# Kernel tuning notes

Hardware: AMD Instinct MI355X
Metric: run time of the kernel (lower is better)

## Reference

```python
import jax, jax.numpy as jnp
import numpy as np

BS, NQ, NK = 4096, 21, 7   # batch, num_neg queries, 7 keys (weekdays)
E = 512                     # key_size == query_size
H = 512                     # hidden_size
NEG_INF = -1e9


def setup_inputs() -> dict:
    key = jax.random.key(0)
    ks = jax.random.split(key, 6)
    sq = 1.0 / np.sqrt(E)
    sh = 1.0 / np.sqrt(H)
    return {
        "queries": jax.random.normal(ks[0], (BS, NQ, E), jnp.float32),
        "keys": jax.random.normal(ks[1], (BS, NK, E), jnp.float32),
        "wq_w": jax.random.normal(ks[2], (H, E), jnp.float32) * sq,
        "wq_b": jnp.zeros((H,), jnp.float32),
        "wk_w": jax.random.normal(ks[3], (H, E), jnp.float32) * sq,
        "wk_b": jnp.zeros((H,), jnp.float32),
        "wv_w": jax.random.normal(ks[4], (1, H), jnp.float32) * sh,
        "wv_b": jnp.zeros((1,), jnp.float32),
        "cum_subs_masks": jax.random.randint(ks[5], (BS, 1, NK, 1), 0, 2).astype(jnp.int32),
        "num_neg": NQ,
    }


def reference(queries, keys, wq_w, wq_b, wk_w, wk_b, wv_w, wv_b, cum_subs_masks, num_neg):
    # dropout p=0.0 -> identity (as in eval / p=0)
    q = jnp.einsum('bqe,he->bqh', queries, wq_w) + wq_b          # (bs,21,H)
    k = jnp.einsum('bke,he->bkh', keys, wk_w) + wk_b             # (bs,7,H)
    # additive score: broadcast q over keys, k over queries
    t = jnp.tanh(q[:, :, None, :] + k[:, None, :, :])            # (bs,21,7,H)
    scores = jnp.einsum('bqkh,oh->bqko', t, wv_w) + wv_b         # (bs,21,7,1)
    scores = scores + cum_subs_masks.astype(scores.dtype) * NEG_INF
    attn_weights = jax.nn.softmax(scores, axis=-2)               # softmax over 7 keys
    # weighted sum of the RAW keys (the module multiplies by expanded `keys`)
    attn_out = jnp.einsum('bqk,bke->bqe', attn_weights[..., 0], keys)  # (bs,21,E)
    return (attn_out, attn_weights)
```

## Files before the change

kernel.cpp:

```cpp
#include <hip/hip_runtime.h>

#define BS_   4096
#define NQ_   21
#define NK_   7
#define E_    512
#define MQ_   (BS_*NQ_)
#define MK_   (BS_*NK_)
#define SCALE_ 2.88539008177792681f

typedef __attribute__((ext_vector_type(8))) short bf16x8;
typedef __attribute__((ext_vector_type(4))) float f32x4;
typedef __attribute__((ext_vector_type(8))) unsigned short u16x8;

__device__ __forceinline__ unsigned int cvt_pk_bf16(float lo, float hi){
  unsigned int r;
  asm("v_cvt_pk_bf16_f32 %0, %1, %2" : "=v"(r) : "v"(lo), "v"(hi));
  return r;
}
__device__ __forceinline__ float bf2f(unsigned short h){
  return __builtin_bit_cast(float, (unsigned int)h << 16);
}
__device__ __forceinline__ void gload_lds16(const void* g, void* l){
  __builtin_amdgcn_global_load_lds(
      (const __attribute__((address_space(1))) unsigned int*)g,
      (__attribute__((address_space(3))) unsigned int*)l, 16, 0, 0);
}

__global__ __launch_bounds__(256) void cast_weights(
    const float* __restrict__ wq, const float* __restrict__ wk,
    unsigned int* __restrict__ oq, unsigned int* __restrict__ ok)
{
  int i = blockIdx.x * 256 + threadIdx.x;
  float4 a = ((const float4*)wq)[i];
  float4 b = ((const float4*)wk)[i];
  uint2 ua = { cvt_pk_bf16(a.x, a.y), cvt_pk_bf16(a.z, a.w) };
  uint2 ub = { cvt_pk_bf16(b.x, b.y), cvt_pk_bf16(b.z, b.w) };
  ((uint2*)oq)[i] = ua;
  ((uint2*)ok)[i] = ub;
}

__global__ __launch_bounds__(256, 2)
void gemm_proj(const float* __restrict__ A, const unsigned short* __restrict__ Bw,
               const float* __restrict__ bias, unsigned short* __restrict__ C, int M)
{
  __shared__ unsigned short Asm[2][128 * 64];
  __shared__ unsigned short Bsm[2][128 * 64];

  const int tid  = threadIdx.x;
  const int lane = tid & 63;
  const int w    = tid >> 6;
  const int wr   = w >> 1, wc = w & 1;

  const int nwg = (M >> 7) << 2;
  int bid = (int)blockIdx.x;
  const int q8 = nwg >> 3;
  bid = (bid & 7) * q8 + (bid >> 3);
  const int  mt = bid >> 2, nt = bid & 3;
  const long m0 = (long)mt << 7;
  const int  n0 = nt << 7;

  const int a_row = tid >> 4;
  const int a_c4  = tid & 15;
  const float* Abase = A + m0 * E_;

  f32x4 acc[4][4];
  const f32x4 z4 = {0.f, 0.f, 0.f, 0.f};
#pragma unroll
  for (int m = 0; m < 4; ++m)
#pragma unroll
    for (int n = 0; n < 4; ++n) acc[m][n] = z4;

  {
#pragma unroll
    for (int i = 0; i < 4; ++i){
      const int tb  = (w << 12) + (i << 10) + (lane << 4);
      const int row = tb >> 7, cb = tb & 127;
      gload_lds16((const char*)Bw + ((n0 + row) << 10) + cb,
                  (char*)Bsm[0] + (w << 12) + (i << 10));
    }
    float4 av[8];
#pragma unroll
    for (int j = 0; j < 8; ++j)
      av[j] = *(const float4*)(Abase + (long)(a_row + j * 16) * E_ + a_c4 * 4);
#pragma unroll
    for (int j = 0; j < 8; ++j){
      uint2 u = { cvt_pk_bf16(av[j].x, av[j].y), cvt_pk_bf16(av[j].z, av[j].w) };
      *(uint2*)&Asm[0][(a_row + j * 16) * 64 + a_c4 * 4] = u;
    }
  }
  __syncthreads();

#pragma unroll
  for (int t = 0; t < 8; ++t){
    const int buf = t & 1, nbuf = buf ^ 1;
    float4 av[8];
    if (t < 7){
      const int k0 = (t + 1) << 6;
#pragma unroll
      for (int i = 0; i < 4; ++i){
        const int tb  = (w << 12) + (i << 10) + (lane << 4);
        const int row = tb >> 7, cb = tb & 127;
        gload_lds16((const char*)Bw + ((n0 + row) << 10) + (k0 << 1) + cb,
                    (char*)Bsm[nbuf] + (w << 12) + (i << 10));
      }
#pragma unroll
      for (int j = 0; j < 8; ++j)
        av[j] = *(const float4*)(Abase + (long)(a_row + j * 16) * E_ + k0 + a_c4 * 4);
    }
#pragma unroll
    for (int kk = 0; kk < 2; ++kk){
      bf16x8 af[4], bfr[4];
#pragma unroll
      for (int m = 0; m < 4; ++m)
        af[m] = *(const bf16x8*)&Asm[buf][(wr * 64 + m * 16 + (lane & 15)) * 64 + kk * 32 + (lane >> 4) * 8];
#pragma unroll
      for (int n = 0; n < 4; ++n)
        bfr[n] = *(const bf16x8*)&Bsm[buf][(wc * 64 + n * 16 + (lane & 15)) * 64 + kk * 32 + (lane >> 4) * 8];
#pragma unroll
      for (int m = 0; m < 4; ++m)
#pragma unroll
        for (int n = 0; n < 4; ++n)
          acc[m][n] = __builtin_amdgcn_mfma_f32_16x16x32_bf16(af[m], bfr[n], acc[m][n], 0, 0, 0);
    }
    if (t < 7){
#pragma unroll
      for (int j = 0; j < 8; ++j){
        uint2 u = { cvt_pk_bf16(av[j].x, av[j].y), cvt_pk_bf16(av[j].z, av[j].w) };
        *(uint2*)&Asm[nbuf][(a_row + j * 16) * 64 + a_c4 * 4] = u;
      }
    }
    __syncthreads();
  }

  const int ccol0 = n0 + wc * 64 + (lane & 15);
  float bvs[4];
#pragma unroll
  for (int n = 0; n < 4; ++n) bvs[n] = bias[ccol0 + n * 16] * SCALE_;
#pragma unroll
  for (int m = 0; m < 4; ++m){
    const long rbase = m0 + wr * 64 + m * 16 + (lane >> 4) * 4;
#pragma unroll
    for (int n = 0; n < 4; ++n){
      const long col = ccol0 + n * 16;
      float v0 = fmaf(acc[m][n][0], SCALE_, bvs[n]);
      float v1 = fmaf(acc[m][n][1], SCALE_, bvs[n]);
      float v2 = fmaf(acc[m][n][2], SCALE_, bvs[n]);
      float v3 = fmaf(acc[m][n][3], SCALE_, bvs[n]);
      unsigned int u01 = cvt_pk_bf16(v0, v1);
      unsigned int u23 = cvt_pk_bf16(v2, v3);
      C[(rbase + 0) * E_ + col] = (unsigned short)(u01 & 0xffffu);
      C[(rbase + 1) * E_ + col] = (unsigned short)(u01 >> 16);
      C[(rbase + 2) * E_ + col] = (unsigned short)(u23 & 0xffffu);
      C[(rbase + 3) * E_ + col] = (unsigned short)(u23 >> 16);
    }
  }
}

__global__ __launch_bounds__(256, 2)
void attn_fused(const unsigned short* __restrict__ qp,
                const unsigned short* __restrict__ kp,
                const float* __restrict__ keys,
                const float* __restrict__ wv, const float* __restrict__ wvb,
                const int* __restrict__ mask,
                float* __restrict__ out0, float* __restrict__ out1)
{
  const int lane = threadIdx.x & 63;
  const int b    = blockIdx.x * 4 + (threadIdx.x >> 6);

  float wvr[8];
  *(float4*)&wvr[0] = ((const float4*)wv)[lane * 2];
  *(float4*)&wvr[4] = ((const float4*)wv)[lane * 2 + 1];

  float kf[NK_][8];
#pragma unroll
  for (int k = 0; k < NK_; ++k){
    u16x8 u = *(const u16x8*)(kp + ((long)b * NK_ + k) * E_ + lane * 8);
#pragma unroll
    for (int j = 0; j < 8; ++j) kf[k][j] = bf2f((unsigned short)u[j]);
  }
  float kr[NK_][8];
#pragma unroll
  for (int k = 0; k < NK_; ++k){
    const float4* p = (const float4*)(keys + ((long)b * NK_ + k) * E_ + lane * 8);
    *(float4*)&kr[k][0] = p[0];
    *(float4*)&kr[k][4] = p[1];
  }

  float wsum = ((wvr[0] + wvr[1]) + (wvr[2] + wvr[3])) + ((wvr[4] + wvr[5]) + (wvr[6] + wvr[7]));
#pragma unroll
  for (int off = 32; off; off >>= 1) wsum += __shfl_xor(wsum, off, 64);

  const float vb = wvb[0];
  float base[NK_];
#pragma unroll
  for (int k = 0; k < NK_; ++k)
    base[k] = (wsum + vb) + (float)mask[b * NK_ + k] * (-1e9f);

  const unsigned short* qrow = qp + (long)b * NQ_ * E_ + lane * 8;
  u16x8 qv = *(const u16x8*)qrow;

  float4* o0 = (float4*)(out0 + (long)b * NQ_ * E_) + lane * 2;
  float*  o1 = out1 + (long)b * (NQ_ * NK_);

  for (int qi = 0; qi < NQ_; ++qi){
    u16x8 qn = qv;
    if (qi < NQ_ - 1) qn = *(const u16x8*)(qrow + (qi + 1) * E_);

    float qf[8];
#pragma unroll
    for (int j = 0; j < 8; ++j) qf[j] = bf2f((unsigned short)qv[j]);
    qv = qn;

    float acc[NK_];
#pragma unroll
    for (int k = 0; k < NK_; ++k){
      float a = 0.f;
#pragma unroll
      for (int j = 0; j < 8; ++j){
        float x = qf[j] + kf[k][j];
        float e = __builtin_amdgcn_exp2f(x);
        float r = __builtin_amdgcn_rcpf(e + 1.0f);
        a = fmaf(wvr[j], r, a);
      }
      acc[k] = a;
    }
#pragma unroll
    for (int k = 0; k < NK_; ++k){
      float a = acc[k];
#pragma unroll
      for (int off = 32; off; off >>= 1) a += __shfl_xor(a, off, 64);
      acc[k] = a;
    }
    float sc[NK_], mx = -3.4e38f;
#pragma unroll
    for (int k = 0; k < NK_; ++k){ sc[k] = fmaf(-2.f, acc[k], base[k]); mx = fmaxf(mx, sc[k]); }
    float sum = 0.f;
#pragma unroll
    for (int k = 0; k < NK_; ++k){ sc[k] = __expf(sc[k] - mx); sum += sc[k]; }
    const float inv = __builtin_amdgcn_rcpf(sum);
    float wgt[NK_];
#pragma unroll
    for (int k = 0; k < NK_; ++k) wgt[k] = sc[k] * inv;

    float wsel = wgt[0];
#pragma unroll
    for (int k = 1; k < NK_; ++k) wsel = (lane == k) ? wgt[k] : wsel;
    if (lane < NK_) o1[qi * NK_ + lane] = wsel;

    float4 lo = {0.f,0.f,0.f,0.f}, hi = {0.f,0.f,0.f,0.f};
#pragma unroll
    for (int k = 0; k < NK_; ++k){
      lo.x = fmaf(wgt[k], kr[k][0], lo.x);
      lo.y = fmaf(wgt[k], kr[k][1], lo.y);
      lo.z = fmaf(wgt[k], kr[k][2], lo.z);
      lo.w = fmaf(wgt[k], kr[k][3], lo.w);
      hi.x = fmaf(wgt[k], kr[k][4], hi.x);
      hi.y = fmaf(wgt[k], kr[k][5], hi.y);
      hi.z = fmaf(wgt[k], kr[k][6], hi.z);
      hi.w = fmaf(wgt[k], kr[k][7], hi.w);
    }
    o0[qi * 128 + 0] = lo;
    o0[qi * 128 + 1] = hi;
  }
}

extern "C" void kernel_launch(void* const* d_in, const int* in_sizes, int n_in,
                              void* d_out, int out_size, void* d_ws, size_t ws_size,
                              hipStream_t stream)
{
  const float* queries = (const float*)d_in[0];
  const float* keys    = (const float*)d_in[1];
  const float* wq_w    = (const float*)d_in[2];
  const float* wq_b    = (const float*)d_in[3];
  const float* wk_w    = (const float*)d_in[4];
  const float* wk_b    = (const float*)d_in[5];
  const float* wv_w    = (const float*)d_in[6];
  const float* wv_b    = (const float*)d_in[7];
  const int*   mask    = (const int*)d_in[8];
  (void)in_sizes; (void)n_in; (void)out_size; (void)ws_size;

  float* out0 = (float*)d_out;
  float* out1 = out0 + (long)MQ_ * E_;

  char* ws = (char*)d_ws;
  unsigned short* wqb = (unsigned short*)ws;
  unsigned short* wkb = (unsigned short*)(ws + 512 * 512 * 2);
  unsigned short* qb  = (unsigned short*)(ws + (1 << 20));
  unsigned short* kb  = qb + (size_t)MQ_ * E_;

  cast_weights<<<dim3(256), dim3(256), 0, stream>>>(wq_w, wk_w, (unsigned int*)wqb, (unsigned int*)wkb);
  gemm_proj<<<dim3((MQ_ / 128) * 4), dim3(256), 0, stream>>>(queries, wqb, wq_b, qb, MQ_);
  gemm_proj<<<dim3((MK_ / 128) * 4), dim3(256), 0, stream>>>(keys,    wkb, wk_b, kb, MK_);
  attn_fused<<<dim3(BS_ / 4), dim3(256), 0, stream>>>(qb, kb, keys, wv_w, wv_b, mask, out0, out1);
}
```

Measured before the change: 302.2 us.

## Merge Q/K projection GEMMs into one launch and drop LDS staging

```diff
diff --git a/kernel.cpp b/kernel.cpp
--- a/kernel.cpp
+++ b/kernel.cpp
@@ -1,4 +1,5 @@
 #include <hip/hip_runtime.h>
+#include <hip/hip_bf16.h>
 
 #define BS_   4096
 #define NQ_   21
@@ -6,62 +7,64 @@
 #define E_    512
 #define MQ_   (BS_*NQ_)
 #define MK_   (BS_*NK_)
+#define MT1_  (MQ_/128)
+#define MT2_  (MK_/128)
 #define SCALE_ 2.88539008177792681f
 
 typedef __attribute__((ext_vector_type(8))) short bf16x8;
 typedef __attribute__((ext_vector_type(4))) float f32x4;
 typedef __attribute__((ext_vector_type(8))) unsigned short u16x8;
 
-__device__ __forceinline__ unsigned int cvt_pk_bf16(float lo, float hi){
-  unsigned int r;
-  asm("v_cvt_pk_bf16_f32 %0, %1, %2" : "=v"(r) : "v"(lo), "v"(hi));
-  return r;
+__device__ __forceinline__ unsigned short f2bfu(float x){
+  return __builtin_bit_cast(unsigned short, __float2bfloat16(x));
 }
 __device__ __forceinline__ float bf2f(unsigned short h){
   return __builtin_bit_cast(float, (unsigned int)h << 16);
 }
-__device__ __forceinline__ void gload_lds16(const void* g, void* l){
-  __builtin_amdgcn_global_load_lds(
-      (const __attribute__((address_space(1))) unsigned int*)g,
-      (__attribute__((address_space(3))) unsigned int*)l, 16, 0, 0);
-}
 
 __global__ __launch_bounds__(256) void cast_weights(
     const float* __restrict__ wq, const float* __restrict__ wk,
-    unsigned int* __restrict__ oq, unsigned int* __restrict__ ok)
+    unsigned short* __restrict__ oq, unsigned short* __restrict__ ok)
 {
   int i = blockIdx.x * 256 + threadIdx.x;
   float4 a = ((const float4*)wq)[i];
   float4 b = ((const float4*)wk)[i];
-  uint2 ua = { cvt_pk_bf16(a.x, a.y), cvt_pk_bf16(a.z, a.w) };
-  uint2 ub = { cvt_pk_bf16(b.x, b.y), cvt_pk_bf16(b.z, b.w) };
-  ((uint2*)oq)[i] = ua;
-  ((uint2*)ok)[i] = ub;
-}
-
-__global__ __launch_bounds__(256, 2)
-void gemm_proj(const float* __restrict__ A, const unsigned short* __restrict__ Bw,
-               const float* __restrict__ bias, unsigned short* __restrict__ C, int M)
-{
-  __shared__ unsigned short Asm[2][128 * 64];
-  __shared__ unsigned short Bsm[2][128 * 64];
-
+  u16x8 u;
+  u[0] = f2bfu(a.x); u[1] = f2bfu(a.y); u[2] = f2bfu(a.z); u[3] = f2bfu(a.w);
+  u[4] = f2bfu(b.x); u[5] = f2bfu(b.y); u[6] = f2bfu(b.z); u[7] = f2bfu(b.w);
+  *(uint2*)(oq + i * 4) = uint2{ (unsigned)u[0] | ((unsigned)u[1] << 16),
+                                 (unsigned)u[2] | ((unsigned)u[3] << 16) };
+  *(uint2*)(ok + i * 4) = uint2{ (unsigned)u[4] | ((unsigned)u[5] << 16),
+                                 (unsigned)u[6] | ((unsigned)u[7] << 16) };
+}
+
+__global__ __launch_bounds__(256)
+void gemm_proj(const float* __restrict__ Aq, const float* __restrict__ Ak,
+               const unsigned short* __restrict__ Bq, const unsigned short* __restrict__ Bk,
+               const float* __restrict__ bq, const float* __restrict__ bk,
+               unsigned short* __restrict__ Cq, unsigned short* __restrict__ Ck)
+{
   const int tid  = threadIdx.x;
   const int lane = tid & 63;
   const int w    = tid >> 6;
   const int wr   = w >> 1, wc = w & 1;
 
-  const int nwg = (M >> 7) << 2;
-  int bid = (int)blockIdx.x;
-  const int q8 = nwg >> 3;
-  bid = (bid & 7) * q8 + (bid >> 3);
-  const int  mt = bid >> 2, nt = bid & 3;
+  const int orig = (int)blockIdx.x;
+  const int j    = orig >> 3;
+  int       mt   = (j >> 2) * 8 + (orig & 7);
+  const int nt   = j & 3;
+
+  const float* A; const unsigned short* Bw; const float* bias; unsigned short* C;
+  if (mt < MT1_){ A = Aq; Bw = Bq; bias = bq; C = Cq; }
+  else          { A = Ak; Bw = Bk; bias = bk; C = Ck; mt -= MT1_; }
+
   const long m0 = (long)mt << 7;
   const int  n0 = nt << 7;
 
-  const int a_row = tid >> 4;
-  const int a_c4  = tid & 15;
-  const float* Abase = A + m0 * E_;
+  const int rA = lane & 15;
+  const int sA = (lane >> 4) * 8;
+  const float*          Ap = A  + (m0 + wr * 64 + rA) * (long)E_ + sA;
+  const unsigned short* Bp = Bw + ((long)(n0 + wc * 64 + rA)) * E_ + sA;
 
   f32x4 acc[4][4];
   const f32x4 z4 = {0.f, 0.f, 0.f, 0.f};
@@ -70,66 +73,35 @@
 #pragma unroll
     for (int n = 0; n < 4; ++n) acc[m][n] = z4;
 
-  {
-#pragma unroll
-    for (int i = 0; i < 4; ++i){
-      const int tb  = (w << 12) + (i << 10) + (lane << 4);
-      const int row = tb >> 7, cb = tb & 127;
-      gload_lds16((const char*)Bw + ((n0 + row) << 10) + cb,
-                  (char*)Bsm[0] + (w << 12) + (i << 10));
-    }
-    float4 av[8];
-#pragma unroll
-    for (int j = 0; j < 8; ++j)
-      av[j] = *(const float4*)(Abase + (long)(a_row + j * 16) * E_ + a_c4 * 4);
-#pragma unroll
-    for (int j = 0; j < 8; ++j){
-      uint2 u = { cvt_pk_bf16(av[j].x, av[j].y), cvt_pk_bf16(av[j].z, av[j].w) };
-      *(uint2*)&Asm[0][(a_row + j * 16) * 64 + a_c4 * 4] = u;
-    }
-  }
-  __syncthreads();
-
-#pragma unroll
+  union U8 { bf16x8 v; unsigned short s[8]; };
+
+#pragma unroll 2
   for (int t = 0; t < 8; ++t){
-    const int buf = t & 1, nbuf = buf ^ 1;
-    float4 av[8];
-    if (t < 7){
-      const int k0 = (t + 1) << 6;
-#pragma unroll
-      for (int i = 0; i < 4; ++i){
-        const int tb  = (w << 12) + (i << 10) + (lane << 4);
-        const int row = tb >> 7, cb = tb & 127;
-        gload_lds16((const char*)Bw + ((n0 + row) << 10) + (k0 << 1) + cb,
-                    (char*)Bsm[nbuf] + (w << 12) + (i << 10));
+#pragma unroll
+    for (int kk = 0; kk < 2; ++kk){
+      const int ko = t * 64 + kk * 32;
+      bf16x8 bfr[4];
+#pragma unroll
+      for (int n = 0; n < 4; ++n)
+        bfr[n] = *(const bf16x8*)(Bp + n * 16 * E_ + ko);
+      bf16x8 af[4];
+#pragma unroll
+      for (int m = 0; m < 4; ++m){
+        float4 lo = *(const float4*)(Ap + m * 16 * E_ + ko);
+        float4 hi = *(const float4*)(Ap + m * 16 * E_ + ko + 4);
+        U8 u;
+        u.s[0] = f2bfu(lo.x); u.s[1] = f2bfu(lo.y);
+        u.s[2] = f2bfu(lo.z); u.s[3] = f2bfu(lo.w);
+        u.s[4] = f2bfu(hi.x); u.s[5] = f2bfu(hi.y);
+        u.s[6] = f2bfu(hi.z); u.s[7] = f2bfu(hi.w);
+        af[m] = u.v;
       }
-#pragma unroll
-      for (int j = 0; j < 8; ++j)
-        av[j] = *(const float4*)(Abase + (long)(a_row + j * 16) * E_ + k0 + a_c4 * 4);
-    }
-#pragma unroll
-    for (int kk = 0; kk < 2; ++kk){
-      bf16x8 af[4], bfr[4];
-#pragma unroll
-      for (int m = 0; m < 4; ++m)
-        af[m] = *(const bf16x8*)&Asm[buf][(wr * 64 + m * 16 + (lane & 15)) * 64 + kk * 32 + (lane >> 4) * 8];
-#pragma unroll
-      for (int n = 0; n < 4; ++n)
-        bfr[n] = *(const bf16x8*)&Bsm[buf][(wc * 64 + n * 16 + (lane & 15)) * 64 + kk * 32 + (lane >> 4) * 8];
 #pragma unroll
       for (int m = 0; m < 4; ++m)
 #pragma unroll
         for (int n = 0; n < 4; ++n)
           acc[m][n] = __builtin_amdgcn_mfma_f32_16x16x32_bf16(af[m], bfr[n], acc[m][n], 0, 0, 0);
     }
-    if (t < 7){
-#pragma unroll
-      for (int j = 0; j < 8; ++j){
-        uint2 u = { cvt_pk_bf16(av[j].x, av[j].y), cvt_pk_bf16(av[j].z, av[j].w) };
-        *(uint2*)&Asm[nbuf][(a_row + j * 16) * 64 + a_c4 * 4] = u;
-      }
-    }
-    __syncthreads();
   }
 
   const int ccol0 = n0 + wc * 64 + (lane & 15);
@@ -142,16 +114,9 @@
 #pragma unroll
     for (int n = 0; n < 4; ++n){
       const long col = ccol0 + n * 16;
-      float v0 = fmaf(acc[m][n][0], SCALE_, bvs[n]);
-      float v1 = fmaf(acc[m][n][1], SCALE_, bvs[n]);
-      float v2 = fmaf(acc[m][n][2], SCALE_, bvs[n]);
-      float v3 = fmaf(acc[m][n][3], SCALE_, bvs[n]);
-      unsigned int u01 = cvt_pk_bf16(v0, v1);
-      unsigned int u23 = cvt_pk_bf16(v2, v3);
-      C[(rbase + 0) * E_ + col] = (unsigned short)(u01 & 0xffffu);
-      C[(rbase + 1) * E_ + col] = (unsigned short)(u01 >> 16);
-      C[(rbase + 2) * E_ + col] = (unsigned short)(u23 & 0xffffu);
-      C[(rbase + 3) * E_ + col] = (unsigned short)(u23 >> 16);
+#pragma unroll
+      for (int jj = 0; jj < 4; ++jj)
+        C[(rbase + jj) * E_ + col] = f2bfu(fmaf(acc[m][n][jj], SCALE_, bvs[n]));
     }
   }
 }
@@ -288,8 +253,8 @@
   unsigned short* qb  = (unsigned short*)(ws + (1 << 20));
   unsigned short* kb  = qb + (size_t)MQ_ * E_;
 
-  cast_weights<<<dim3(256), dim3(256), 0, stream>>>(wq_w, wk_w, (unsigned int*)wqb, (unsigned int*)wkb);
-  gemm_proj<<<dim3((MQ_ / 128) * 4), dim3(256), 0, stream>>>(queries, wqb, wq_b, qb, MQ_);
-  gemm_proj<<<dim3((MK_ / 128) * 4), dim3(256), 0, stream>>>(keys,    wkb, wk_b, kb, MK_);
+  cast_weights<<<dim3(256), dim3(256), 0, stream>>>(wq_w, wk_w, wqb, wkb);
+  gemm_proj<<<dim3((MT1_ + MT2_) * 4), dim3(256), 0, stream>>>(
+      queries, keys, wqb, wkb, wq_b, wk_b, qb, kb);
   attn_fused<<<dim3(BS_ / 4), dim3(256), 0, stream>>>(qb, kb, keys, wv_w, wv_b, mask, out0, out1);
 }
```

Measured after the change: 440.0 us. +45.6%, slower.

## Merge Q/K projection GEMMs into one launch and XOR-swizzle LDS tiles

Applied to the files above, without the earlier changes.

```diff
diff --git a/kernel.cpp b/kernel.cpp
--- a/kernel.cpp
+++ b/kernel.cpp
@@ -6,6 +6,8 @@
 #define E_    512
 #define MQ_   (BS_*NQ_)
 #define MK_   (BS_*NK_)
+#define MT1_  (MQ_/128)
+#define MT2_  (MK_/128)
 #define SCALE_ 2.88539008177792681f
 
 typedef __attribute__((ext_vector_type(8))) short bf16x8;
@@ -40,8 +42,10 @@
 }
 
 __global__ __launch_bounds__(256, 2)
-void gemm_proj(const float* __restrict__ A, const unsigned short* __restrict__ Bw,
-               const float* __restrict__ bias, unsigned short* __restrict__ C, int M)
+void gemm_proj(const float* __restrict__ Aq, const float* __restrict__ Ak,
+               const unsigned short* __restrict__ Bq, const unsigned short* __restrict__ Bk,
+               const float* __restrict__ bq, const float* __restrict__ bk,
+               unsigned short* __restrict__ Cq, unsigned short* __restrict__ Ck)
 {
   __shared__ unsigned short Asm[2][128 * 64];
   __shared__ unsigned short Bsm[2][128 * 64];
@@ -51,17 +55,36 @@
   const int w    = tid >> 6;
   const int wr   = w >> 1, wc = w & 1;
 
-  const int nwg = (M >> 7) << 2;
-  int bid = (int)blockIdx.x;
-  const int q8 = nwg >> 3;
-  bid = (bid & 7) * q8 + (bid >> 3);
-  const int  mt = bid >> 2, nt = bid & 3;
+  const int orig = (int)blockIdx.x;
+  const int j    = orig >> 3;
+  int       mt   = (j >> 2) * 8 + (orig & 7);
+  const int nt   = j & 3;
+
+  const float* A; const unsigned short* Bw; const float* bias; unsigned short* C;
+  if (mt < MT1_){ A = Aq; Bw = Bq; bias = bq; C = Cq; }
+  else          { A = Ak; Bw = Bk; bias = bk; C = Ck; mt -= MT1_; }
+
   const long m0 = (long)mt << 7;
   const int  n0 = nt << 7;
 
+  long bsrc[4];
+#pragma unroll
+  for (int i = 0; i < 4; ++i){
+    const int tb  = (w << 12) + (i << 10) + (lane << 4);
+    const int row = tb >> 7;
+    const int cb  = (tb & 127) ^ ((row & 7) << 4);
+    bsrc[i] = ((long)(n0 + row) << 10) + cb;
+  }
+
   const int a_row = tid >> 4;
   const int a_c4  = tid & 15;
+  const int awoff = (a_c4 * 8) ^ ((a_row & 7) << 4);
   const float* Abase = A + m0 * E_;
+
+  const int rbyteA = (wr * 64 + (lane & 15)) * 128;
+  const int rbyteB = (wc * 64 + (lane & 15)) * 128;
+  const int kxor0  = (((lane >> 4) * 16) +  0) ^ ((lane & 7) << 4);
+  const int kxor1  = (((lane >> 4) * 16) + 64) ^ ((lane & 7) << 4);
 
   f32x4 acc[4][4];
   const f32x4 z4 = {0.f, 0.f, 0.f, 0.f};
@@ -72,20 +95,17 @@
 
   {
 #pragma unroll
-    for (int i = 0; i < 4; ++i){
-      const int tb  = (w << 12) + (i << 10) + (lane << 4);
-      const int row = tb >> 7, cb = tb & 127;
-      gload_lds16((const char*)Bw + ((n0 + row) << 10) + cb,
+    for (int i = 0; i < 4; ++i)
+      gload_lds16((const char*)Bw + bsrc[i],
                   (char*)Bsm[0] + (w << 12) + (i << 10));
-    }
     float4 av[8];
 #pragma unroll
-    for (int j = 0; j < 8; ++j)
-      av[j] = *(const float4*)(Abase + (long)(a_row + j * 16) * E_ + a_c4 * 4);
-#pragma unroll
-    for (int j = 0; j < 8; ++j){
-      uint2 u = { cvt_pk_bf16(av[j].x, av[j].y), cvt_pk_bf16(av[j].z, av[j].w) };
-      *(uint2*)&Asm[0][(a_row + j * 16) * 64 + a_c4 * 4] = u;
+    for (int jj = 0; jj < 8; ++jj)
+      av[jj] = *(const float4*)(Abase + (long)(a_row + jj * 16) * E_ + a_c4 * 4);
+#pragma unroll
+    for (int jj = 0; jj < 8; ++jj){
+      uint2 u = { cvt_pk_bf16(av[jj].x, av[jj].y), cvt_pk_bf16(av[jj].z, av[jj].w) };
+      *(uint2*)((char*)Asm[0] + (a_row + jj * 16) * 128 + awoff) = u;
     }
   }
   __syncthreads();
@@ -97,25 +117,23 @@
     if (t < 7){
       const int k0 = (t + 1) << 6;
 #pragma unroll
-      for (int i = 0; i < 4; ++i){
-        const int tb  = (w << 12) + (i << 10) + (lane << 4);
-        const int row = tb >> 7, cb = tb & 127;
-        gload_lds16((const char*)Bw + ((n0 + row) << 10) + (k0 << 1) + cb,
+      for (int i = 0; i < 4; ++i)
+        gload_lds16((const char*)Bw + bsrc[i] + (k0 << 1),
                     (char*)Bsm[nbuf] + (w << 12) + (i << 10));
-      }
-#pragma unroll
-      for (int j = 0; j < 8; ++j)
-        av[j] = *(const float4*)(Abase + (long)(a_row + j * 16) * E_ + k0 + a_c4 * 4);
+#pragma unroll
+      for (int jj = 0; jj < 8; ++jj)
+        av[jj] = *(const float4*)(Abase + (long)(a_row + jj * 16) * E_ + k0 + a_c4 * 4);
     }
 #pragma unroll
     for (int kk = 0; kk < 2; ++kk){
+      const int kx = kk ? kxor1 : kxor0;
       bf16x8 af[4], bfr[4];
 #pragma unroll
       for (int m = 0; m < 4; ++m)
-        af[m] = *(const bf16x8*)&Asm[buf][(wr * 64 + m * 16 + (lane & 15)) * 64 + kk * 32 + (lane >> 4) * 8];
+        af[m] = *(const bf16x8*)((const char*)Asm[buf] + rbyteA + m * 2048 + kx);
 #pragma unroll
       for (int n = 0; n < 4; ++n)
-        bfr[n] = *(const bf16x8*)&Bsm[buf][(wc * 64 + n * 16 + (lane & 15)) * 64 + kk * 32 + (lane >> 4) * 8];
+        bfr[n] = *(const bf16x8*)((const char*)Bsm[buf] + rbyteB + n * 2048 + kx);
 #pragma unroll
       for (int m = 0; m < 4; ++m)
 #pragma unroll
@@ -124,9 +142,9 @@
     }
     if (t < 7){
 #pragma unroll
-      for (int j = 0; j < 8; ++j){
-        uint2 u = { cvt_pk_bf16(av[j].x, av[j].y), cvt_pk_bf16(av[j].z, av[j].w) };
-        *(uint2*)&Asm[nbuf][(a_row + j * 16) * 64 + a_c4 * 4] = u;
+      for (int jj = 0; jj < 8; ++jj){
+        uint2 u = { cvt_pk_bf16(av[jj].x, av[jj].y), cvt_pk_bf16(av[jj].z, av[jj].w) };
+        *(uint2*)((char*)Asm[nbuf] + (a_row + jj * 16) * 128 + awoff) = u;
       }
     }
     __syncthreads();
@@ -289,7 +307,7 @@
   unsigned short* kb  = qb + (size_t)MQ_ * E_;
 
   cast_weights<<<dim3(256), dim3(256), 0, stream>>>(wq_w, wk_w, (unsigned int*)wqb, (unsigned int*)wkb);
-  gemm_proj<<<dim3((MQ_ / 128) * 4), dim3(256), 0, stream>>>(queries, wqb, wq_b, qb, MQ_);
-  gemm_proj<<<dim3((MK_ / 128) * 4), dim3(256), 0, stream>>>(keys,    wkb, wk_b, kb, MK_);
+  gemm_proj<<<dim3((MT1_ + MT2_) * 4), dim3(256), 0, stream>>>(
+      queries, keys, wqb, wkb, wq_b, wk_b, qb, kb);
   attn_fused<<<dim3(BS_ / 4), dim3(256), 0, stream>>>(qb, kb, keys, wv_w, wv_b, mask, out0, out1);
 }
```

New measurement: 268.5 us. -11.1%, faster.
